# Performance work log

Measured on AMD Instinct MI355X. Metric: run time of the kernel, lower is better.

## Reference

```python
import jax, jax.numpy as jnp
import numpy as np

B, S, D, H = 2, 2048, 2048, 16
HD = D // H  # 128


def _rope(t, cos, sin):
    # t: [B, S, H, HD]; cos/sin: [S, HD//2]
    te, to = t[..., ::2], t[..., 1::2]
    c = cos[None, :, None, :]
    s = sin[None, :, None, :]
    re = te * c - to * s
    im = te * s + to * c
    # interleave back (matches tf.stack(..., axis=-1) + reshape)
    return jnp.stack([re, im], axis=-1).reshape(t.shape)


def setup_inputs() -> dict:
    key = jax.random.key(0)
    ks = jax.random.split(key, 6)
    x = jax.random.normal(ks[0], (B, S, D), dtype=jnp.float32)
    Wq = jax.random.normal(ks[1], (D, D), dtype=jnp.float32) * 0.02
    Wk = jax.random.normal(ks[2], (D, D), dtype=jnp.float32) * 0.02
    Wv = jax.random.normal(ks[3], (D, D), dtype=jnp.float32) * 0.02
    Wo = jax.random.normal(ks[4], (D, D), dtype=jnp.float32) * 0.02
    # rotary embeddings: freqs_cis = exp(i * pos * inv_freq)
    inv_freq = 1.0 / (10000.0 ** (jnp.arange(0, HD, 2, dtype=jnp.float32) / HD))  # [HD//2]
    angles = jnp.arange(S, dtype=jnp.float32)[:, None] * inv_freq[None, :]  # [S, HD//2]
    freqs_cos = jnp.cos(angles)
    freqs_sin = jnp.sin(angles)
    # additive causal mask [1,1,S,S]
    causal = jnp.tril(jnp.ones((S, S), dtype=bool))
    mask = jnp.where(causal, 0.0, -1e9).astype(jnp.float32)[None, None]
    return {"x": x, "Wq": Wq, "Wk": Wk, "Wv": Wv, "Wo": Wo,
            "freqs_cos": freqs_cos, "freqs_sin": freqs_sin, "mask": mask}


def reference(x, Wq, Wk, Wv, Wo, freqs_cos, freqs_sin, mask):
    b, s, d = x.shape
    xq = (x @ Wq).reshape(b, s, H, HD)
    xk = (x @ Wk).reshape(b, s, H, HD)
    xv = (x @ Wv).reshape(b, s, H, HD)
    xq = _rope(xq, freqs_cos, freqs_sin)
    xk = _rope(xk, freqs_cos, freqs_sin)
    # [B, H, S, HD]
    xq = xq.transpose(0, 2, 1, 3)
    xk = xk.transpose(0, 2, 1, 3)
    xv = xv.transpose(0, 2, 1, 3)
    scores = jnp.einsum('bhqd,bhkd->bhqk', xq, xk) / jnp.sqrt(jnp.float32(HD))
    scores = scores + mask[:, :, :s, :s]
    probs = jax.nn.softmax(scores + 1e-9, axis=-1)
    out = jnp.einsum('bhqk,bhkd->bhqd', probs, xv)
    out = out.transpose(0, 2, 1, 3).reshape(b, s, d)
    return out @ Wo
```

## Files before the change

kernel.cpp:

```cpp
#include <hip/hip_runtime.h>
#include <cstdint>

#define BB 2
#define SS 2048
#define DD 2048
#define HH 16
#define HDIM 128
#define MM (BB * SS)

typedef __attribute__((ext_vector_type(8))) short bf16x8;
typedef __attribute__((ext_vector_type(4))) short bf16x4;
typedef __attribute__((ext_vector_type(4))) float f32x4;
typedef __attribute__((ext_vector_type(16))) float f32x16;

__device__ inline short f2bf(float f) {
  union { float f; unsigned u; } v; v.f = f;
  unsigned r = v.u + 0x7FFFu + ((v.u >> 16) & 1u);
  return (short)(r >> 16);
}
__device__ inline float bf2f(short s) {
  union { float f; unsigned u; } v;
  v.u = ((unsigned)(unsigned short)s) << 16;
  return v.f;
}
__device__ inline float asf(int u) { union { int i; float f; } v; v.i = u; return v.f; }
__device__ inline int asi(float f) { union { float f; int i; } v; v.f = f; return v.i; }

__device__ inline unsigned cvtpk_bf16(float lo, float hi) {
  unsigned r;
  asm("v_cvt_pk_bf16_f32 %0, %1, %2" : "=v"(r) : "v"(lo), "v"(hi));
  return r;
}

__device__ inline void gll16(const void* g, void* l) {
  __builtin_amdgcn_global_load_lds(
      (const __attribute__((address_space(1))) void*)g,
      (__attribute__((address_space(3))) void*)l, 16, 0, 0);
}

__global__ __launch_bounds__(256) void cast_bf16_kernel(
    const float* __restrict__ x, short* __restrict__ y, int n4) {
  int i = blockIdx.x * 256 + threadIdx.x;
  if (i >= n4) return;
  float4 v = reinterpret_cast<const float4*>(x)[i];
  bf16x4 o;
  o[0] = f2bf(v.x); o[1] = f2bf(v.y); o[2] = f2bf(v.z); o[3] = f2bf(v.w);
  reinterpret_cast<bf16x4*>(y)[i] = o;
}

__global__ __launch_bounds__(256) void transpose4_kernel(
    const float* __restrict__ Wq, const float* __restrict__ Wk,
    const float* __restrict__ Wv, const float* __restrict__ Wo,
    short* __restrict__ WqkvT, short* __restrict__ WoT) {
  __shared__ short tile[64][65];
  int z = blockIdx.z;
  const float* W = (z == 0) ? Wq : (z == 1) ? Wk : (z == 2) ? Wv : Wo;
  short* Wt = (z < 3) ? (WqkvT + (size_t)z * DD * DD) : WoT;
  int c = threadIdx.x & 63, r4 = threadIdx.x >> 6;
  int n0 = blockIdx.x << 6, k0 = blockIdx.y << 6;
#pragma unroll
  for (int p = 0; p < 16; ++p) {
    int r = (p << 2) + r4;
    tile[c][r] = f2bf(W[(size_t)(k0 + r) * DD + n0 + c]);
  }
  __syncthreads();
#pragma unroll
  for (int p = 0; p < 16; ++p) {
    int r = (p << 2) + r4;
    Wt[(size_t)(n0 + r) * DD + k0 + c] = tile[r][c];
  }
}

__global__ __launch_bounds__(256) void transpose_v_kernel(
    const short* __restrict__ V, short* __restrict__ Vt) {
  __shared__ short tile[64][65];
  int c = threadIdx.x & 63, r4 = threadIdx.x >> 6;
  int s0 = blockIdx.x << 6, d0 = blockIdx.y << 6;
  int bh = blockIdx.z;
  int b = bh >> 4, h = bh & 15;
#pragma unroll
  for (int p = 0; p < 16; ++p) {
    int r = (p << 2) + r4;
    tile[c][r] = V[(size_t)(b * SS + s0 + r) * DD + h * HDIM + d0 + c];
  }
  __syncthreads();
#pragma unroll
  for (int p = 0; p < 16; ++p) {
    int r = (p << 2) + r4;
    Vt[((size_t)bh * HDIM + d0 + r) * SS + s0 + c] = tile[r][c];
  }
}

template <int BN, int MODE>
__global__ __launch_bounds__(512) void gemm8_kernel(
    const short* __restrict__ A, const short* __restrict__ Bt,
    short* __restrict__ Qb, short* __restrict__ Kb, short* __restrict__ Vb,
    float* __restrict__ Cf,
    const float* __restrict__ fc, const float* __restrict__ fs) {
  constexpr int FN = BN / 32;
  constexpr int LB = BN / 64;
  constexpr int BH = BN * 32;
  __shared__ short smem[2][16384 + BN * 64];

  const int tid = threadIdx.x;
  const int lane = tid & 63, w = tid >> 6;
  const int cl = lane & 15, gq = lane >> 4;
  const int wm = w >> 1, wn = w & 1;

  const int bid = blockIdx.x;
  const int xcd = bid & 7, local = bid >> 3;
  constexpr int TNX = (BN == 192) ? 4 : 2;
  const int tm = local & 15, tn = xcd * TNX + (local >> 4);
  const int m0 = tm << 8, n0 = tn * BN;

  f32x4 acc[4][FN];
#pragma unroll
  for (int i = 0; i < 4; ++i)
#pragma unroll
    for (int j = 0; j < FN; ++j) {
      f32x4 z = {0.f, 0.f, 0.f, 0.f};
      acc[i][j] = z;
    }

  auto stageA = [&](int t, int l, short* buf) {
    int D = l * 8192 + tid * 16;
    int half = D >> 14;
    int row = (D >> 6) & 255;
    int p2 = (D >> 4) & 3;
    int col = t * 64 + half * 32 + ((p2 ^ (row & 3)) << 3);
    gll16(&A[(size_t)(m0 + row) * DD + col], (char*)buf + D);
  };
  auto stageB = [&](int t, int l, short* buf) {
    int D = l * 8192 + tid * 16;
    int half = (D >= BN * 64) ? 1 : 0;
    int row = (D - half * BN * 64) >> 6;
    int p2 = (D >> 4) & 3;
    int col = t * 64 + half * 32 + ((p2 ^ (row & 3)) << 3);
    gll16(&Bt[(size_t)(n0 + row) * DD + col], (char*)buf + 32768 + D);
  };

  auto compute = [&](const short* base, int ks) {
    const short* Ab = base;
    const short* Bb = base + 16384;
    bf16x8 af[4], bfv[FN];
#pragma unroll
    for (int fm = 0; fm < 4; ++fm) {
      int ra = wm * 64 + fm * 16 + cl;
      af[fm] = *reinterpret_cast<const bf16x8*>(
          &Ab[ks * 8192 + ra * 32 + ((gq ^ (ra & 3)) << 3)]);
    }
#pragma unroll
    for (int fn = 0; fn < FN; ++fn) {
      int rb = wn * (BN / 2) + fn * 16 + cl;
      bfv[fn] = *reinterpret_cast<const bf16x8*>(
          &Bb[ks * BH + rb * 32 + ((gq ^ (rb & 3)) << 3)]);
    }
    __builtin_amdgcn_s_setprio(1);
#pragma unroll
    for (int fm = 0; fm < 4; ++fm)
#pragma unroll
      for (int fn = 0; fn < FN; ++fn)
        acc[fm][fn] = __builtin_amdgcn_mfma_f32_16x16x32_bf16(
            af[fm], bfv[fn], acc[fm][fn], 0, 0, 0);
    __builtin_amdgcn_s_setprio(0);
  };

  stageA(0, 0, smem[0]); stageA(0, 1, smem[0]);
#pragma unroll
  for (int l = 0; l < LB; ++l) stageB(0, l, smem[0]);
  stageA(0, 2, smem[0]); stageA(0, 3, smem[0]);
  asm volatile("s_waitcnt vmcnt(2)" ::: "memory");
  __builtin_amdgcn_s_barrier();

  for (int t = 0; t < 31; ++t) {
    short* cur = smem[t & 1];
    short* nxt = smem[(t + 1) & 1];
    stageA(t + 1, 0, nxt); stageA(t + 1, 1, nxt);
#pragma unroll
    for (int l = 0; l < LB; ++l) stageB(t + 1, l, nxt);
    compute(cur, 0);
    if constexpr (BN == 192)
      asm volatile("s_waitcnt vmcnt(5)" ::: "memory");
    else
      asm volatile("s_waitcnt vmcnt(4)" ::: "memory");
    __builtin_amdgcn_s_barrier();
    stageA(t + 1, 2, nxt); stageA(t + 1, 3, nxt);
    compute(cur, 1);
    asm volatile("s_waitcnt vmcnt(2)" ::: "memory");
    __builtin_amdgcn_s_barrier();
  }
  compute(smem[1], 0);
  asm volatile("s_waitcnt vmcnt(0)" ::: "memory");
  __builtin_amdgcn_s_barrier();
  compute(smem[1], 1);

  if constexpr (MODE == 0) {
#pragma unroll
    for (int fm = 0; fm < 4; ++fm)
#pragma unroll
      for (int r = 0; r < 4; ++r) {
        int mrow = m0 + wm * 64 + fm * 16 + gq * 4 + r;
        int s = mrow & (SS - 1);
#pragma unroll
        for (int fn = 0; fn < FN; ++fn) {
          int ncol = n0 + wn * (BN / 2) + fn * 16 + cl;
          float v = acc[fm][fn][r];
          float vp = __shfl_xor(v, 1, 64);
          if (ncol < 4096) {
            int c = ncol & 127;
            int i = c >> 1;
            float cv = fc[s * 64 + i], sv = fs[s * 64 + i];
            float o = (c & 1) ? (v * cv + vp * sv) : (v * cv - vp * sv);
            float qs = (ncol < 2048) ? 0.127517448f : 1.0f;
            short* Dp = (ncol < 2048) ? Qb : Kb;
            Dp[(size_t)mrow * DD + (ncol & (DD - 1))] = f2bf(o * qs);
          } else {
            Vb[(size_t)mrow * DD + (ncol - 4096)] = f2bf(v);
          }
        }
      }
  } else {
#pragma unroll
    for (int fm = 0; fm < 4; ++fm)
#pragma unroll
      for (int r = 0; r < 4; ++r) {
        int mrow = m0 + wm * 64 + fm * 16 + gq * 4 + r;
#pragma unroll
        for (int fn = 0; fn < FN; ++fn) {
          int ncol = n0 + wn * (BN / 2) + fn * 16 + cl;
          Cf[(size_t)mrow * DD + ncol] = acc[fm][fn][r];
        }
      }
  }
}

__global__ __launch_bounds__(256, 2) void attn_kernel(
    const short* __restrict__ Q, const short* __restrict__ K,
    const short* __restrict__ Vt, short* __restrict__ O) {
  __shared__ short Kl[2][64 * 128];
  __shared__ short Vl[2][128 * 64];
  const int id = blockIdx.x;
  const int qi = 15 - (id >> 5);
  const int bh = id & 31;
  const int b = bh >> 4, h = bh & 15;
  const int tid = threadIdx.x;
  const int lane = tid & 63, w = tid >> 6;
  const int l31 = lane & 31, hi = lane >> 5;
  const int qw = qi * 128 + w * 32;
  const int qg = qw + l31;

  const short* Kbase = K + (size_t)b * SS * DD + h * HDIM;
  const short* Vbase = Vt + (size_t)bh * HDIM * SS;
  int krow[4], kq[4], vd[4], vs[4];
#pragma unroll
  for (int i = 0; i < 4; ++i) {
    int c = w * 4 + i;
    krow[i] = c * 4 + (lane >> 4);
    kq[i] = (lane & 15) ^ (krow[i] & 7);
    vd[i] = c * 8 + (lane >> 3);
    vs[i] = (lane & 7) ^ (vd[i] & 7);
  }

  bf16x8 qf[8];
  const size_t qoff = ((size_t)b * SS + qg) * DD + h * HDIM;
#pragma unroll
  for (int s = 0; s < 8; ++s)
    qf[s] = *reinterpret_cast<const bf16x8*>(&Q[qoff + s * 16 + hi * 8]);

  f32x16 ot[4];
#pragma unroll
  for (int dt = 0; dt < 4; ++dt)
#pragma unroll
    for (int r = 0; r < 16; ++r) ot[dt][r] = 0.f;
  float m_run = -INFINITY, l_run = 0.f;

  const int NT = 2 * qi + 2;

#pragma unroll
  for (int i = 0; i < 4; ++i) {
    gll16(Kbase + (size_t)krow[i] * DD + kq[i] * 8, &Kl[0][(w * 4 + i) * 512]);
    gll16(Vbase + (size_t)vd[i] * SS + vs[i] * 8, &Vl[0][(w * 4 + i) * 512]);
  }
  __syncthreads();

  for (int t = 0; t < NT; ++t) {
    const int cur = t & 1;
    if (t + 1 < NT) {
      const int nt64 = (t + 1) * 64;
#pragma unroll
      for (int i = 0; i < 4; ++i) {
        gll16(Kbase + (size_t)(nt64 + krow[i]) * DD + kq[i] * 8,
              &Kl[cur ^ 1][(w * 4 + i) * 512]);
        gll16(Vbase + (size_t)vd[i] * SS + nt64 + vs[i] * 8,
              &Vl[cur ^ 1][(w * 4 + i) * 512]);
      }
    }

    if (t * 64 <= qw + 31) {
      const short* Kc = Kl[cur];
      const short* Vc = Vl[cur];
      f32x16 st0, st1;
#pragma unroll
      for (int r = 0; r < 16; ++r) { st0[r] = 0.f; st1[r] = 0.f; }
      __builtin_amdgcn_s_setprio(1);
#pragma unroll
      for (int s = 0; s < 8; ++s) {
        const int cs = (s * 2 + hi);
        bf16x8 kf0 = *reinterpret_cast<const bf16x8*>(
            &Kc[l31 * 128 + ((cs ^ (l31 & 7)) << 3)]);
        st0 = __builtin_amdgcn_mfma_f32_32x32x16_bf16(kf0, qf[s], st0, 0, 0, 0);
        bf16x8 kf1 = *reinterpret_cast<const bf16x8*>(
            &Kc[(32 + l31) * 128 + ((cs ^ (l31 & 7)) << 3)]);
        st1 = __builtin_amdgcn_mfma_f32_32x32x16_bf16(kf1, qf[s], st1, 0, 0, 0);
      }
      __builtin_amdgcn_s_setprio(0);
      if (t * 64 + 63 > qw) {
#pragma unroll
        for (int r = 0; r < 16; ++r) {
          int dl = (r & 3) + 8 * (r >> 2) + 4 * hi;
          if (t * 64 + dl > qg) st0[r] = -1e30f;
          if (t * 64 + 32 + dl > qg) st1[r] = -1e30f;
        }
      }
      float mx[16];
#pragma unroll
      for (int r = 0; r < 16; ++r) mx[r] = fmaxf(st0[r], st1[r]);
#pragma unroll
      for (int off = 8; off >= 1; off >>= 1)
#pragma unroll
        for (int r = 0; r < 8; ++r)
          if (r < off) mx[r] = fmaxf(mx[r], mx[r + off]);
      float pm = mx[0];
      {
        auto sw = __builtin_amdgcn_permlane32_swap(asi(pm), asi(pm), false, false);
        pm = fmaxf(asf(sw[0]), asf(sw[1]));
      }
      if (!__all(pm <= m_run + 11.5f)) {
        float mn = fmaxf(m_run, pm);
        float al = exp2f(m_run - mn);
        m_run = mn;
        l_run *= al;
#pragma unroll
        for (int dt = 0; dt < 4; ++dt)
#pragma unroll
          for (int r = 0; r < 16; ++r) ot[dt][r] *= al;
      }
#pragma unroll
      for (int r = 0; r < 16; ++r) st0[r] = exp2f(st0[r] - m_run);
#pragma unroll
      for (int r = 0; r < 16; ++r) st1[r] = exp2f(st1[r] - m_run);
      float sm[16];
#pragma unroll
      for (int r = 0; r < 16; ++r) sm[r] = st0[r] + st1[r];
#pragma unroll
      for (int off = 8; off >= 1; off >>= 1)
#pragma unroll
        for (int r = 0; r < 8; ++r)
          if (r < off) sm[r] += sm[r + off];
      float ps = sm[0];
      {
        auto sw = __builtin_amdgcn_permlane32_swap(asi(ps), asi(ps), false, false);
        ps = asf(sw[0]) + asf(sw[1]);
      }
      l_run += ps;

      bf16x8 pf[4];
#pragma unroll
      for (int s = 0; s < 4; ++s) {
        float e0, e1, e2, e3, e4, e5, e6, e7;
        if (s < 2) {
          e0 = st0[8 * s + 0]; e1 = st0[8 * s + 1]; e2 = st0[8 * s + 2]; e3 = st0[8 * s + 3];
          e4 = st0[8 * s + 4]; e5 = st0[8 * s + 5]; e6 = st0[8 * s + 6]; e7 = st0[8 * s + 7];
        } else {
          e0 = st1[8 * (s - 2) + 0]; e1 = st1[8 * (s - 2) + 1]; e2 = st1[8 * (s - 2) + 2]; e3 = st1[8 * (s - 2) + 3];
          e4 = st1[8 * (s - 2) + 4]; e5 = st1[8 * (s - 2) + 5]; e6 = st1[8 * (s - 2) + 6]; e7 = st1[8 * (s - 2) + 7];
        }
        unsigned a0 = cvtpk_bf16(e0, e1);
        unsigned a1 = cvtpk_bf16(e2, e3);
        unsigned b0 = cvtpk_bf16(e4, e5);
        unsigned b1 = cvtpk_bf16(e6, e7);
        auto r0 = __builtin_amdgcn_permlane32_swap((int)a0, (int)b0, false, false);
        auto r1 = __builtin_amdgcn_permlane32_swap((int)a1, (int)b1, false, false);
        union { int u[4]; bf16x8 v; } pk;
        pk.u[0] = r0[0]; pk.u[1] = r1[0]; pk.u[2] = r0[1]; pk.u[3] = r1[1];
        pf[s] = pk.v;
      }

      __builtin_amdgcn_s_setprio(1);
#pragma unroll
      for (int dt = 0; dt < 4; ++dt) {
        const int vr = dt * 32 + l31;
#pragma unroll
        for (int s = 0; s < 4; ++s) {
          bf16x8 vf = *reinterpret_cast<const bf16x8*>(
              &Vc[vr * 64 + (((s * 2 + hi) ^ (vr & 7)) << 3)]);
          ot[dt] = __builtin_amdgcn_mfma_f32_32x32x16_bf16(vf, pf[s], ot[dt], 0, 0, 0);
        }
      }
      __builtin_amdgcn_s_setprio(0);
    }
    __syncthreads();
  }

  float inv = 1.0f / l_run;
  const size_t orow = ((size_t)b * SS + qg) * DD + h * HDIM;
#pragma unroll
  for (int dt = 0; dt < 4; ++dt)
#pragma unroll
    for (int g = 0; g < 4; ++g) {
      bf16x4 v;
#pragma unroll
      for (int k = 0; k < 4; ++k) v[k] = f2bf(ot[dt][4 * g + k] * inv);
      *reinterpret_cast<bf16x4*>(&O[orow + dt * 32 + 8 * g + 4 * hi]) = v;
    }
}

extern "C" void kernel_launch(void* const* d_in, const int* in_sizes, int n_in,
                              void* d_out, int out_size, void* d_ws, size_t ws_size,
                              hipStream_t stream) {
  const float* x = (const float*)d_in[0];
  const float* Wq = (const float*)d_in[1];
  const float* Wk = (const float*)d_in[2];
  const float* Wv = (const float*)d_in[3];
  const float* Wo = (const float*)d_in[4];
  const float* fc = (const float*)d_in[5];
  const float* fs = (const float*)d_in[6];
  float* out = (float*)d_out;
  char* ws = (char*)d_ws;

  short* xb     = (short*)(ws + 0);
  short* WqkvT  = (short*)(ws + (size_t)16 * 1048576);
  short* WoT    = (short*)(ws + (size_t)40 * 1048576);
  short* Qb     = (short*)(ws + (size_t)48 * 1048576);
  short* Kb     = (short*)(ws + (size_t)64 * 1048576);
  short* Vb     = (short*)(ws + (size_t)80 * 1048576);
  short* VtB    = WqkvT;

  cast_bf16_kernel<<<8192, 256, 0, stream>>>(x, xb, 2097152);
  transpose4_kernel<<<dim3(32, 32, 4), 256, 0, stream>>>(Wq, Wk, Wv, Wo, WqkvT, WoT);

  gemm8_kernel<192, 0><<<512, 512, 0, stream>>>(
      xb, WqkvT, Qb, Kb, Vb, nullptr, fc, fs);

  transpose_v_kernel<<<dim3(32, 2, 32), 256, 0, stream>>>(Vb, VtB);

  attn_kernel<<<512, 256, 0, stream>>>(Qb, Kb, VtB, xb);

  gemm8_kernel<128, 1><<<256, 512, 0, stream>>>(
      xb, WoT, nullptr, nullptr, nullptr, out, nullptr, nullptr);
}
```

Measured before the change: 281.9 us.

## Rewrite GEMM kernel with larger 256x256 tiles, 2x4 wave grid, new swizzle

Replaces the 256xBN GEMM with a templated BMxBN kernel. Waves are laid out 2x4, LDS rows are 64-wide with an XOR-8 swizzle, and global loads for the next K-tile are issued inside the compute loop, with one __syncthreads per tile replacing the hand-tuned vmcnt waits. The QKV projection now uses 256x256 tiles over 384 blocks and the output projection uses 128x256 tiles. Larger tiles raise data reuse per block. In exchange the QKV launch has fewer blocks for 256 CUs, the kernel needs more LDS and registers, and the simpler synchronisation may expose load latency.

```diff
diff --git a/kernel.cpp b/kernel.cpp
--- a/kernel.cpp
+++ b/kernel.cpp
@@ -91,144 +91,144 @@
   }
 }
 
-template <int BN, int MODE>
-__global__ __launch_bounds__(512) void gemm8_kernel(
+template <int BM, int BN, int ND, int MODE>
+__global__ __launch_bounds__(512) void gemm_big_kernel(
     const short* __restrict__ A, const short* __restrict__ Bt,
     short* __restrict__ Qb, short* __restrict__ Kb, short* __restrict__ Vb,
     float* __restrict__ Cf,
     const float* __restrict__ fc, const float* __restrict__ fs) {
-  constexpr int FN = BN / 32;
-  constexpr int LB = BN / 64;
-  constexpr int BH = BN * 32;
-  __shared__ short smem[2][16384 + BN * 64];
+  constexpr int WTM = BM / 2, WTN = BN / 4;
+  constexpr int FM = WTM / 16, FN = WTN / 16;
+  constexpr int LA = BM / 64, LB = BN / 64;
+  constexpr int ASZ = BM * 64;
+  constexpr int BSZ = BN * 64;
+  __shared__ short smem[2][ASZ + BSZ];
 
   const int tid = threadIdx.x;
   const int lane = tid & 63, w = tid >> 6;
   const int cl = lane & 15, gq = lane >> 4;
-  const int wm = w >> 1, wn = w & 1;
-
-  const int bid = blockIdx.x;
-  const int xcd = bid & 7, local = bid >> 3;
-  constexpr int TNX = (BN == 192) ? 4 : 2;
-  const int tm = local & 15, tn = xcd * TNX + (local >> 4);
-  const int m0 = tm << 8, n0 = tn * BN;
-
-  f32x4 acc[4][FN];
-#pragma unroll
-  for (int i = 0; i < 4; ++i)
+  const int wm = w >> 2, wn = w & 3;
+
+  constexpr int TMC = 4096 / BM;
+  constexpr int TNX = (ND / BN) / 8;
+  const int xcd = blockIdx.x & 7, local = blockIdx.x >> 3;
+  const int tm = local % TMC, tn = xcd * TNX + local / TMC;
+  const int m0 = tm * BM, n0 = tn * BN;
+
+  f32x4 acc[FM][FN];
+#pragma unroll
+  for (int i = 0; i < FM; ++i)
 #pragma unroll
     for (int j = 0; j < FN; ++j) {
       f32x4 z = {0.f, 0.f, 0.f, 0.f};
       acc[i][j] = z;
     }
 
-  auto stageA = [&](int t, int l, short* buf) {
-    int D = l * 8192 + tid * 16;
-    int half = D >> 14;
-    int row = (D >> 6) & 255;
-    int p2 = (D >> 4) & 3;
-    int col = t * 64 + half * 32 + ((p2 ^ (row & 3)) << 3);
-    gll16(&A[(size_t)(m0 + row) * DD + col], (char*)buf + D);
+  const int srow = lane >> 3;
+  const int sseg = lane & 7;
+
+  auto stageA = [&](int t, int b, int j) {
+    int row = j * 64 + w * 8 + srow;
+    int sg = sseg ^ (row & 7);
+    gll16(&A[(size_t)(m0 + row) * DD + t * 64 + sg * 8],
+          &smem[b][(j * 64 + w * 8) * 64]);
   };
-  auto stageB = [&](int t, int l, short* buf) {
-    int D = l * 8192 + tid * 16;
-    int half = (D >= BN * 64) ? 1 : 0;
-    int row = (D - half * BN * 64) >> 6;
-    int p2 = (D >> 4) & 3;
-    int col = t * 64 + half * 32 + ((p2 ^ (row & 3)) << 3);
-    gll16(&Bt[(size_t)(n0 + row) * DD + col], (char*)buf + 32768 + D);
+  auto stageB = [&](int t, int b, int j) {
+    int row = j * 64 + w * 8 + srow;
+    int sg = sseg ^ (row & 7);
+    gll16(&Bt[(size_t)(n0 + row) * DD + t * 64 + sg * 8],
+          &smem[b][ASZ + (j * 64 + w * 8) * 64]);
   };
 
-  auto compute = [&](const short* base, int ks) {
-    const short* Ab = base;
-    const short* Bb = base + 16384;
-    bf16x8 af[4], bfv[FN];
-#pragma unroll
-    for (int fm = 0; fm < 4; ++fm) {
-      int ra = wm * 64 + fm * 16 + cl;
-      af[fm] = *reinterpret_cast<const bf16x8*>(
-          &Ab[ks * 8192 + ra * 32 + ((gq ^ (ra & 3)) << 3)]);
+#pragma unroll
+  for (int j = 0; j < LA; ++j) stageA(0, 0, j);
+#pragma unroll
+  for (int j = 0; j < LB; ++j) stageB(0, 0, j);
+  __syncthreads();
+
+  for (int t = 0; t < 32; ++t) {
+    const short* Ab = smem[t & 1];
+    const short* Bb = Ab + ASZ;
+    const int nb = (t + 1) & 1;
+    const bool more = (t + 1 < 32);
+#pragma unroll
+    for (int ks = 0; ks < 2; ++ks) {
+      bf16x8 bh[FN];
+#pragma unroll
+      for (int mq = 0; mq < 2; ++mq) {
+        if (ks == 0 && mq == 0 && more) {
+#pragma unroll
+          for (int j = 0; j < LA; ++j) stageA(t + 1, nb, j);
+        }
+        if (ks == 0 && mq == 1 && more) {
+#pragma unroll
+          for (int j = 0; j < LB; ++j) stageB(t + 1, nb, j);
+        }
+        bf16x8 af[FM / 2];
+#pragma unroll
+        for (int f = 0; f < FM / 2; ++f) {
+          int ra = wm * WTM + mq * (WTM / 2) + f * 16 + cl;
+          af[f] = *reinterpret_cast<const bf16x8*>(
+              &Ab[ra * 64 + (((ks * 4 + gq) ^ (ra & 7)) << 3)]);
+        }
+        if (mq == 0) {
+#pragma unroll
+          for (int fn = 0; fn < FN; ++fn) {
+            int rb = wn * WTN + fn * 16 + cl;
+            bh[fn] = *reinterpret_cast<const bf16x8*>(
+                &Bb[rb * 64 + (((ks * 4 + gq) ^ (rb & 7)) << 3)]);
+          }
+        }
+        __builtin_amdgcn_s_setprio(1);
+#pragma unroll
+        for (int f = 0; f < FM / 2; ++f)
+#pragma unroll
+          for (int fn = 0; fn < FN; ++fn)
+            acc[mq * (FM / 2) + f][fn] = __builtin_amdgcn_mfma_f32_16x16x32_bf16(
+                af[f], bh[fn], acc[mq * (FM / 2) + f][fn], 0, 0, 0);
+        __builtin_amdgcn_s_setprio(0);
+      }
     }
-#pragma unroll
-    for (int fn = 0; fn < FN; ++fn) {
-      int rb = wn * (BN / 2) + fn * 16 + cl;
-      bfv[fn] = *reinterpret_cast<const bf16x8*>(
-          &Bb[ks * BH + rb * 32 + ((gq ^ (rb & 3)) << 3)]);
-    }
-    __builtin_amdgcn_s_setprio(1);
-#pragma unroll
-    for (int fm = 0; fm < 4; ++fm)
-#pragma unroll
-      for (int fn = 0; fn < FN; ++fn)
-        acc[fm][fn] = __builtin_amdgcn_mfma_f32_16x16x32_bf16(
-            af[fm], bfv[fn], acc[fm][fn], 0, 0, 0);
-    __builtin_amdgcn_s_setprio(0);
-  };
-
-  stageA(0, 0, smem[0]); stageA(0, 1, smem[0]);
-#pragma unroll
-  for (int l = 0; l < LB; ++l) stageB(0, l, smem[0]);
-  stageA(0, 2, smem[0]); stageA(0, 3, smem[0]);
-  asm volatile("s_waitcnt vmcnt(2)" ::: "memory");
-  __builtin_amdgcn_s_barrier();
-
-  for (int t = 0; t < 31; ++t) {
-    short* cur = smem[t & 1];
-    short* nxt = smem[(t + 1) & 1];
-    stageA(t + 1, 0, nxt); stageA(t + 1, 1, nxt);
-#pragma unroll
-    for (int l = 0; l < LB; ++l) stageB(t + 1, l, nxt);
-    compute(cur, 0);
-    if constexpr (BN == 192)
-      asm volatile("s_waitcnt vmcnt(5)" ::: "memory");
-    else
-      asm volatile("s_waitcnt vmcnt(4)" ::: "memory");
-    __builtin_amdgcn_s_barrier();
-    stageA(t + 1, 2, nxt); stageA(t + 1, 3, nxt);
-    compute(cur, 1);
-    asm volatile("s_waitcnt vmcnt(2)" ::: "memory");
-    __builtin_amdgcn_s_barrier();
-  }
-  compute(smem[1], 0);
-  asm volatile("s_waitcnt vmcnt(0)" ::: "memory");
-  __builtin_amdgcn_s_barrier();
-  compute(smem[1], 1);
+    __syncthreads();
+  }
 
   if constexpr (MODE == 0) {
-#pragma unroll
-    for (int fm = 0; fm < 4; ++fm)
+    const int mat = tn >> 3;
+    const int cbase = (tn & 7) * BN + wn * WTN;
+#pragma unroll
+    for (int fm = 0; fm < FM; ++fm)
 #pragma unroll
       for (int r = 0; r < 4; ++r) {
-        int mrow = m0 + wm * 64 + fm * 16 + gq * 4 + r;
+        int mrow = m0 + wm * WTM + fm * 16 + gq * 4 + r;
         int s = mrow & (SS - 1);
 #pragma unroll
         for (int fn = 0; fn < FN; ++fn) {
-          int ncol = n0 + wn * (BN / 2) + fn * 16 + cl;
+          int col = cbase + fn * 16 + cl;
           float v = acc[fm][fn][r];
-          float vp = __shfl_xor(v, 1, 64);
-          if (ncol < 4096) {
-            int c = ncol & 127;
+          if (mat < 2) {
+            int c = col & 127;
             int i = c >> 1;
             float cv = fc[s * 64 + i], sv = fs[s * 64 + i];
+            float vp = __shfl_xor(v, 1, 64);
             float o = (c & 1) ? (v * cv + vp * sv) : (v * cv - vp * sv);
-            float qs = (ncol < 2048) ? 0.127517448f : 1.0f;
-            short* Dp = (ncol < 2048) ? Qb : Kb;
-            Dp[(size_t)mrow * DD + (ncol & (DD - 1))] = f2bf(o * qs);
+            float qs = (mat == 0) ? 0.127517448f : 1.0f;
+            short* Dp = (mat == 0) ? Qb : Kb;
+            Dp[(size_t)mrow * DD + col] = f2bf(o * qs);
           } else {
-            Vb[(size_t)mrow * DD + (ncol - 4096)] = f2bf(v);
+            Vb[(size_t)mrow * DD + col] = f2bf(v);
           }
         }
       }
   } else {
 #pragma unroll
-    for (int fm = 0; fm < 4; ++fm)
+    for (int fm = 0; fm < FM; ++fm)
 #pragma unroll
       for (int r = 0; r < 4; ++r) {
-        int mrow = m0 + wm * 64 + fm * 16 + gq * 4 + r;
+        int mrow = m0 + wm * WTM + fm * 16 + gq * 4 + r;
 #pragma unroll
         for (int fn = 0; fn < FN; ++fn) {
-          int ncol = n0 + wn * (BN / 2) + fn * 16 + cl;
-          Cf[(size_t)mrow * DD + ncol] = acc[fm][fn][r];
+          int ncol = n0 + wn * WTN + fn * 16 + cl;
+          Cf[(size_t)mrow * ND + ncol] = acc[fm][fn][r];
         }
       }
   }
@@ -439,13 +439,13 @@
   cast_bf16_kernel<<<8192, 256, 0, stream>>>(x, xb, 2097152);
   transpose4_kernel<<<dim3(32, 32, 4), 256, 0, stream>>>(Wq, Wk, Wv, Wo, WqkvT, WoT);
 
-  gemm8_kernel<192, 0><<<512, 512, 0, stream>>>(
+  gemm_big_kernel<256, 256, 6144, 0><<<384, 512, 0, stream>>>(
       xb, WqkvT, Qb, Kb, Vb, nullptr, fc, fs);
 
   transpose_v_kernel<<<dim3(32, 2, 32), 256, 0, stream>>>(Vb, VtB);
 
   attn_kernel<<<512, 256, 0, stream>>>(Qb, Kb, VtB, xb);
 
-  gemm8_kernel<128, 1><<<256, 512, 0, stream>>>(
+  gemm_big_kernel<128, 256, 2048, 1><<<256, 512, 0, stream>>>(
       xb, WoT, nullptr, nullptr, nullptr, out, nullptr, nullptr);
 }
```

New measurement: 302.7 us. 1.07x slower.
